# Kernel tuning notes

Hardware: AMD Instinct MI355X
Metric: run time of the kernel (lower is better)

Reference implementation:

```python
import jax, jax.numpy as jnp
import numpy as np

H = 16
QK_DIM = 1024
EPS = 1e-5


def setup_inputs() -> dict:
    key = jax.random.key(0)
    ks = jax.random.split(key, 5)
    B, N, M, D = 2, 2048, 2048, 1024
    x = jax.random.normal(ks[0], (B, N, D), jnp.float32)
    context = jax.random.normal(ks[1], (B, M, D), jnp.float32)
    Wq = jax.random.normal(ks[2], (QK_DIM, D), jnp.float32) * (D ** -0.5)
    Wkv = jax.random.normal(ks[3], (QK_DIM + 1024, D), jnp.float32) * (D ** -0.5)
    Wtalk = jax.random.normal(ks[4], (H, H), jnp.float32) * (H ** -0.5)
    ln_gamma = jnp.ones((H,), jnp.float32)
    ln_beta = jnp.zeros((H,), jnp.float32)
    return {"x": x, "context": context, "Wq": Wq, "Wkv": Wkv,
            "Wtalk": Wtalk, "ln_gamma": ln_gamma, "ln_beta": ln_beta}


def _split_heads(t):
    # b n (h d) -> b h n d
    b, n, hd = t.shape
    return t.reshape(b, n, H, hd // H).transpose(0, 2, 1, 3)


def reference(x, context, Wq, Wkv, Wtalk, ln_gamma, ln_beta):
    q = x @ Wq.T                      # [B,N,QK]
    kv = context @ Wkv.T              # [B,M,QK+V]
    k, v = kv[..., :QK_DIM], kv[..., QK_DIM:]
    q, k, v = _split_heads(q), _split_heads(k), _split_heads(v)
    q = q * (q.shape[-1] ** -0.5)
    scores = jnp.einsum('bhid,bhjd->bhij', q, k)          # [B,H,N,M]
    aw = jax.nn.softmax(scores, axis=-1)
    # talking heads: Linear over head axis then LayerNorm over head axis
    aw = jnp.einsum('bhij,gh->bgij', aw, Wtalk)
    mu = jnp.mean(aw, axis=1, keepdims=True)
    var = jnp.var(aw, axis=1, keepdims=True)
    aw = (aw - mu) * jax.lax.rsqrt(var + EPS)
    aw = aw * ln_gamma[None, :, None, None] + ln_beta[None, :, None, None]
    attn = jnp.einsum('bhij,bhjd->bhid', aw, v)           # [B,H,N,dv]
    b, h, n, d = attn.shape
    return attn.transpose(0, 2, 1, 3).reshape(b, n, h * d)  # [B,N,V]
```

## Files before the change

### kernel.cpp

```cpp
#include <hip/hip_runtime.h>


typedef __attribute__((ext_vector_type(8))) short short8;
typedef __attribute__((ext_vector_type(4))) short short4v;
typedef __attribute__((ext_vector_type(4))) float float4v;
typedef unsigned short u16;

#define MFMA16(a, b, c) __builtin_amdgcn_mfma_f32_16x16x32_bf16((a), (b), (c), 0, 0, 0)

__device__ inline u16 f2bf(float f) {
  unsigned u = __float_as_uint(f);
  u += 0x7FFFu + ((u >> 16) & 1u);
  return (u16)(u >> 16);
}

__global__ __launch_bounds__(256) void cast_bf16(const float* __restrict__ in,
                                                 u16* __restrict__ out, int n) {
  int i = (blockIdx.x * 256 + threadIdx.x) * 8;
  if (i + 8 > n) return;
  float4v f0 = *(const float4v*)(in + i);
  float4v f1 = *(const float4v*)(in + i + 4);
  short8 o;
  o[0] = (short)f2bf(f0[0]); o[1] = (short)f2bf(f0[1]);
  o[2] = (short)f2bf(f0[2]); o[3] = (short)f2bf(f0[3]);
  o[4] = (short)f2bf(f1[0]); o[5] = (short)f2bf(f1[1]);
  o[6] = (short)f2bf(f1[2]); o[7] = (short)f2bf(f1[3]);
  *(short8*)(out + i) = o;
}

template <int MODE>
__global__ __launch_bounds__(256, 4) void gemm_bt(const u16* __restrict__ A,
                                                  const u16* __restrict__ W,
                                                  u16* __restrict__ out0,
                                                  u16* __restrict__ out1) {
  __shared__ u16 As[64][40];
  __shared__ u16 Ws[64][40];
  const int t = threadIdx.x;
  const int wave = t >> 6, l = t & 63, l15 = l & 15, lq = l >> 4;
  const int r0 = blockIdx.x * 64, c0 = blockIdx.y * 64;
  const int srow = t >> 2, sch = t & 3;
  const u16* ag = A + (r0 + srow) * 1024 + sch * 8;
  const u16* wg = W + (c0 + srow) * 1024 + sch * 8;

  float4v acc[4];
#pragma unroll
  for (int i = 0; i < 4; ++i) acc[i] = (float4v){0.f, 0.f, 0.f, 0.f};

  short8 av = *(const short8*)ag;
  short8 wv = *(const short8*)wg;
  for (int kt = 0; kt < 32; ++kt) {
    __syncthreads();
    *(short8*)&As[srow][sch * 8] = av;
    *(short8*)&Ws[srow][sch * 8] = wv;
    __syncthreads();
    if (kt < 31) {
      av = *(const short8*)(ag + (kt + 1) * 32);
      wv = *(const short8*)(wg + (kt + 1) * 32);
    }
    short8 af = *(const short8*)&As[wave * 16 + l15][lq * 8];
#pragma unroll
    for (int fn = 0; fn < 4; ++fn) {
      short8 bf = *(const short8*)&Ws[fn * 16 + l15][lq * 8];
      acc[fn] = MFMA16(af, bf, acc[fn]);
    }
  }
#pragma unroll
  for (int fn = 0; fn < 4; ++fn) {
#pragma unroll
    for (int r = 0; r < 4; ++r) {
      int row = r0 + wave * 16 + lq * 4 + r;
      int col = c0 + fn * 16 + l15;
      int b = row >> 11, n = row & 2047;
      float v = acc[fn][r];
      if (MODE == 0) {
        v *= 0.125f;
        int h = col >> 6, d = col & 63;
        out0[(((b * 16 + h) * 2048 + n) << 6) + d] = f2bf(v);
      } else {
        if (col < 1024) {
          int h = col >> 6, d = col & 63;
          out0[(((b * 16 + h) * 2048 + n) << 6) + d] = f2bf(v);
        } else {
          int cc = col - 1024;
          int h = cc >> 6, d = cc & 63;
          out1[(((b * 16 + h) * 2048 + n) << 6) + d] = f2bf(v);
        }
      }
    }
  }
}

__global__ __launch_bounds__(256) void transpose_v(const u16* __restrict__ vh,
                                                   u16* __restrict__ vt) {
  __shared__ u16 tile[64][72];
  const int t = threadIdx.x;
  const int j0 = blockIdx.x * 64, h = blockIdx.y, b = blockIdx.z;
  const u16* src = vh + (((b * 16 + h) * 2048 + j0) << 6);
  int row = t >> 2, c = t & 3;
  short8 v0 = *(const short8*)(src + row * 64 + c * 8);
  short8 v1 = *(const short8*)(src + row * 64 + (c + 4) * 8);
  *(short8*)&tile[row][c * 8] = v0;
  *(short8*)&tile[row][(c + 4) * 8] = v1;
  __syncthreads();
  int d = t >> 2, jc = t & 3;
  short8 o0, o1;
#pragma unroll
  for (int jj = 0; jj < 8; ++jj) o0[jj] = (short)tile[jc * 16 + jj][d];
#pragma unroll
  for (int jj = 0; jj < 8; ++jj) o1[jj] = (short)tile[jc * 16 + 8 + jj][d];
  u16* dst = vt + ((b * 16 + h) * 64 + d) * 2048 + j0 + jc * 16;
  *(short8*)dst = o0;
  *(short8*)(dst + 8) = o1;
}

__global__ __launch_bounds__(1024) void attn_fused(
    const u16* __restrict__ qh, const u16* __restrict__ kh,
    const u16* __restrict__ vt, const float* __restrict__ wtalk,
    const float* __restrict__ gamma, const float* __restrict__ beta,
    float* __restrict__ out) {
  __shared__ u16 P_lds[2][512 * 36];
  __shared__ u16 Y_lds[2][16 * 16 * 36];

  const int tid = threadIdx.x;
  const int wv = tid >> 6;
  const int l = tid & 63, l15 = l & 15, lq = l >> 4;
  const int i0 = blockIdx.x * 16;
  const int b = blockIdx.y;
  const int bh = b * 16 + wv;

  {
    u16* pz = &P_lds[0][0];
    for (int z = tid; z < 2 * 512 * 36; z += 1024) pz[z] = 0;
  }

  short8 wfrag;
#pragma unroll
  for (int t8 = 0; t8 < 8; ++t8) {
    int h = lq * 8 + t8;
    float wval = (h < 16) ? wtalk[l15 * 16 + h] : 0.f;
    wfrag[t8] = (short)f2bf(wval);
  }
  float gam[4], bet[4];
#pragma unroll
  for (int r = 0; r < 4; ++r) {
    gam[r] = gamma[lq * 4 + r];
    bet[r] = beta[lq * 4 + r];
  }

  const u16* qbase = qh + ((bh * 2048 + i0) << 6);
  short8 qf0 = *(const short8*)(qbase + l15 * 64 + lq * 8);
  short8 qf1 = *(const short8*)(qbase + l15 * 64 + 32 + lq * 8);
  const u16* kbase = kh + ((bh * 2048) << 6);
  const u16* vbase = vt + (bh * 64) * 2048;

  __syncthreads();

  float ps0 = 0.f, ps1 = 0.f, ps2 = 0.f, ps3 = 0.f;
  short8 k00 = *(const short8*)(kbase + l15 * 64 + lq * 8);
  short8 k01 = *(const short8*)(kbase + l15 * 64 + 32 + lq * 8);
  short8 k10 = *(const short8*)(kbase + (16 + l15) * 64 + lq * 8);
  short8 k11 = *(const short8*)(kbase + (16 + l15) * 64 + 32 + lq * 8);
  for (int jt = 0; jt < 64; ++jt) {
    short8 n00, n01, n10, n11;
    if (jt < 63) {
      const u16* kp = kbase + (((jt + 1) * 32) << 6);
      n00 = *(const short8*)(kp + l15 * 64 + lq * 8);
      n01 = *(const short8*)(kp + l15 * 64 + 32 + lq * 8);
      n10 = *(const short8*)(kp + (16 + l15) * 64 + lq * 8);
      n11 = *(const short8*)(kp + (16 + l15) * 64 + 32 + lq * 8);
    }
    float4v s0 = {0.f, 0.f, 0.f, 0.f}, s1 = {0.f, 0.f, 0.f, 0.f};
    s0 = MFMA16(qf0, k00, s0);
    s0 = MFMA16(qf1, k01, s0);
    s1 = MFMA16(qf0, k10, s1);
    s1 = MFMA16(qf1, k11, s1);
    ps0 += __expf(s0[0]) + __expf(s1[0]);
    ps1 += __expf(s0[1]) + __expf(s1[1]);
    ps2 += __expf(s0[2]) + __expf(s1[2]);
    ps3 += __expf(s0[3]) + __expf(s1[3]);
    k00 = n00; k01 = n01; k10 = n10; k11 = n11;
  }
#pragma unroll
  for (int d = 1; d < 16; d <<= 1) {
    ps0 += __shfl_xor(ps0, d);
    ps1 += __shfl_xor(ps1, d);
    ps2 += __shfl_xor(ps2, d);
    ps3 += __shfl_xor(ps3, d);
  }
  float bc[4];
  bc[0] = -logf(ps0); bc[1] = -logf(ps1);
  bc[2] = -logf(ps2); bc[3] = -logf(ps3);

  float4v acc0 = {0.f, 0.f, 0.f, 0.f}, acc1 = acc0, acc2 = acc0, acc3 = acc0;
  short8 kc00 = *(const short8*)(kbase + l15 * 64 + lq * 8);
  short8 kc01 = *(const short8*)(kbase + l15 * 64 + 32 + lq * 8);
  short8 kc10 = *(const short8*)(kbase + (16 + l15) * 64 + lq * 8);
  short8 kc11 = *(const short8*)(kbase + (16 + l15) * 64 + 32 + lq * 8);
  short8 v0, v1, v2, v3;

  for (int jt = 0; jt <= 64; ++jt) {
    const int buf = jt & 1, pbuf = (jt - 1) & 1;
    if (jt >= 1) {
      const u16* vp = vbase + (jt - 1) * 32 + lq * 8;
      v0 = *(const short8*)(vp + (l15) * 2048);
      v1 = *(const short8*)(vp + (16 + l15) * 2048);
      v2 = *(const short8*)(vp + (32 + l15) * 2048);
      v3 = *(const short8*)(vp + (48 + l15) * 2048);
    }
    short8 kn00, kn01, kn10, kn11;
    if (jt + 1 < 64) {
      const u16* kp = kbase + (((jt + 1) * 32) << 6);
      kn00 = *(const short8*)(kp + l15 * 64 + lq * 8);
      kn01 = *(const short8*)(kp + l15 * 64 + 32 + lq * 8);
      kn10 = *(const short8*)(kp + (16 + l15) * 64 + lq * 8);
      kn11 = *(const short8*)(kp + (16 + l15) * 64 + 32 + lq * 8);
    }
    if (jt < 64) {
      float4v s0 = {0.f, 0.f, 0.f, 0.f}, s1 = {0.f, 0.f, 0.f, 0.f};
      s0 = MFMA16(qf0, kc00, s0);
      s0 = MFMA16(qf1, kc01, s0);
      s1 = MFMA16(qf0, kc10, s1);
      s1 = MFMA16(qf1, kc11, s1);
      int ebase = (lq * 4) * 32 + l15;
#pragma unroll
      for (int r = 0; r < 4; ++r) {
        float p0 = __expf(s0[r] + bc[r]);
        float p1 = __expf(s1[r] + bc[r]);
        P_lds[buf][(ebase + r * 32) * 36 + wv] = f2bf(p0);
        P_lds[buf][(ebase + r * 32 + 16) * 36 + wv] = f2bf(p1);
      }
    }
    __syncthreads();
    if (jt < 64) {
      float4v t0 = {0.f, 0.f, 0.f, 0.f}, t1 = {0.f, 0.f, 0.f, 0.f};
      {
        int e00 = wv * 32 + l15;
        int e10 = wv * 32 + 16 + l15;
        const u16* p0p = &P_lds[buf][e00 * 36 + lq * 8];
        const u16* p1p = &P_lds[buf][e10 * 36 + lq * 8];
        short4v x0 = *(const short4v*)p0p;
        short4v x1 = *(const short4v*)(p0p + 4);
        short4v y0 = *(const short4v*)p1p;
        short4v y1 = *(const short4v*)(p1p + 4);
        short8 pb0 = __builtin_shufflevector(x0, x1, 0, 1, 2, 3, 4, 5, 6, 7);
        short8 pb1 = __builtin_shufflevector(y0, y1, 0, 1, 2, 3, 4, 5, 6, 7);
        t0 = MFMA16(wfrag, pb0, t0);
        t1 = MFMA16(wfrag, pb1, t1);
      }
#pragma unroll
      for (int c2 = 0; c2 < 2; ++c2) {
        float4v tt = c2 ? t1 : t0;
        float sum = tt[0] + tt[1] + tt[2] + tt[3];
        sum += __shfl_xor(sum, 16);
        sum += __shfl_xor(sum, 32);
        float mu = sum * 0.0625f;
        float ss = tt[0] * tt[0] + tt[1] * tt[1] + tt[2] * tt[2] + tt[3] * tt[3];
        ss += __shfl_xor(ss, 16);
        ss += __shfl_xor(ss, 32);
        float var = ss * 0.0625f - mu * mu;
        float rs = rsqrtf(var + 1e-5f);
#pragma unroll
        for (int r = 0; r < 4; ++r) {
          float y = (tt[r] - mu) * rs * gam[r] + bet[r];
          Y_lds[buf][((lq * 4 + r) * 16 + wv) * 36 + c2 * 16 + l15] = f2bf(y);
        }
      }
    }
    if (jt >= 1) {
      short8 yf = *(const short8*)&Y_lds[pbuf][(wv * 16 + l15) * 36 + lq * 8];
      acc0 = MFMA16(yf, v0, acc0);
      acc1 = MFMA16(yf, v1, acc1);
      acc2 = MFMA16(yf, v2, acc2);
      acc3 = MFMA16(yf, v3, acc3);
    }
    kc00 = kn00; kc01 = kn01; kc10 = kn10; kc11 = kn11;
  }
  float* ob = out + (b * 2048 + i0) * 1024 + wv * 64;
#pragma unroll
  for (int r = 0; r < 4; ++r) {
    float* orow = ob + (lq * 4 + r) * 1024;
    orow[l15] = acc0[r];
    orow[16 + l15] = acc1[r];
    orow[32 + l15] = acc2[r];
    orow[48 + l15] = acc3[r];
  }
}

extern "C" void kernel_launch(void* const* d_in, const int* in_sizes, int n_in,
                              void* d_out, int out_size, void* d_ws,
                              size_t ws_size, hipStream_t stream) {
  const float* x = (const float*)d_in[0];
  const float* ctx = (const float*)d_in[1];
  const float* Wq = (const float*)d_in[2];
  const float* Wkv = (const float*)d_in[3];
  const float* Wtalk = (const float*)d_in[4];
  const float* gam = (const float*)d_in[5];
  const float* bet = (const float*)d_in[6];
  float* out = (float*)d_out;

  u16* xb = (u16*)d_ws;
  u16* cb = xb + 4194304;
  u16* wqb = cb + 4194304;
  u16* wkvb = wqb + 1048576;
  u16* qhb = wkvb + 2097152;
  u16* khb = qhb + 4194304;
  u16* vhb = khb + 4194304;
  u16* vtb = vhb + 4194304;

  cast_bf16<<<2048, 256, 0, stream>>>(x, xb, 4194304);
  cast_bf16<<<2048, 256, 0, stream>>>(ctx, cb, 4194304);
  cast_bf16<<<512, 256, 0, stream>>>(Wq, wqb, 1048576);
  cast_bf16<<<1024, 256, 0, stream>>>(Wkv, wkvb, 2097152);

  gemm_bt<0><<<dim3(64, 16), 256, 0, stream>>>(xb, wqb, qhb, nullptr);
  gemm_bt<1><<<dim3(64, 32), 256, 0, stream>>>(cb, wkvb, khb, vhb);

  transpose_v<<<dim3(32, 16, 2), 256, 0, stream>>>(vhb, vtb);

  attn_fused<<<dim3(128, 2), 1024, 0, stream>>>(qhb, khb, vtb, Wtalk, gam, bet,
                                                out);
}
```

Measured before the change: 507.1 us.

## Split attention into denominator and pass-2 kernels with key-range split-K and atomics

The fused attention kernel becomes two kernels. The first computes softmax denominators over half the key range per block and accumulates them with atomicAdd. The second does the probability, talking-heads and layernorm, and PV pass per key half, accumulating output with atomics into a memset buffer. This doubles the grid so more CUs are busy. It also folds log2e into the Q scale so exp2 can be used, and shrinks the talking-heads MFMA to a K=16 variant with a smaller P buffer. The cost is extra memsets, float atomics on the output, and nondeterministic summation order.

```diff
diff --git a/kernel.cpp b/kernel.cpp
--- a/kernel.cpp
+++ b/kernel.cpp
@@ -7,12 +7,15 @@
 typedef unsigned short u16;
 
 #define MFMA16(a, b, c) __builtin_amdgcn_mfma_f32_16x16x32_bf16((a), (b), (c), 0, 0, 0)
+#define MFMA16K16(a, b, c) __builtin_amdgcn_mfma_f32_16x16x16bf16_1k((a), (b), (c), 0, 0, 0)
 
 __device__ inline u16 f2bf(float f) {
   unsigned u = __float_as_uint(f);
   u += 0x7FFFu + ((u >> 16) & 1u);
   return (u16)(u >> 16);
 }
+
+__device__ inline float fexp2(float x) { return __builtin_amdgcn_exp2f(x); }
 
 __global__ __launch_bounds__(256) void cast_bf16(const float* __restrict__ in,
                                                  u16* __restrict__ out, int n) {
@@ -73,7 +76,7 @@
       int b = row >> 11, n = row & 2047;
       float v = acc[fn][r];
       if (MODE == 0) {
-        v *= 0.125f;
+        v *= 0.125f * 1.44269504088896f;
         int h = col >> 6, d = col & 63;
         out0[(((b * 16 + h) * 2048 + n) << 6) + d] = f2bf(v);
       } else {
@@ -113,56 +116,30 @@
   *(short8*)(dst + 8) = o1;
 }
 
-__global__ __launch_bounds__(1024) void attn_fused(
+__global__ __launch_bounds__(1024, 8) void attn_denom(
     const u16* __restrict__ qh, const u16* __restrict__ kh,
-    const u16* __restrict__ vt, const float* __restrict__ wtalk,
-    const float* __restrict__ gamma, const float* __restrict__ beta,
-    float* __restrict__ out) {
-  __shared__ u16 P_lds[2][512 * 36];
-  __shared__ u16 Y_lds[2][16 * 16 * 36];
-
+    float* __restrict__ lsum) {
   const int tid = threadIdx.x;
   const int wv = tid >> 6;
   const int l = tid & 63, l15 = l & 15, lq = l >> 4;
   const int i0 = blockIdx.x * 16;
-  const int b = blockIdx.y;
+  const int jh = blockIdx.y;
+  const int b = blockIdx.z;
   const int bh = b * 16 + wv;
-
-  {
-    u16* pz = &P_lds[0][0];
-    for (int z = tid; z < 2 * 512 * 36; z += 1024) pz[z] = 0;
-  }
-
-  short8 wfrag;
-#pragma unroll
-  for (int t8 = 0; t8 < 8; ++t8) {
-    int h = lq * 8 + t8;
-    float wval = (h < 16) ? wtalk[l15 * 16 + h] : 0.f;
-    wfrag[t8] = (short)f2bf(wval);
-  }
-  float gam[4], bet[4];
-#pragma unroll
-  for (int r = 0; r < 4; ++r) {
-    gam[r] = gamma[lq * 4 + r];
-    bet[r] = beta[lq * 4 + r];
-  }
 
   const u16* qbase = qh + ((bh * 2048 + i0) << 6);
   short8 qf0 = *(const short8*)(qbase + l15 * 64 + lq * 8);
   short8 qf1 = *(const short8*)(qbase + l15 * 64 + 32 + lq * 8);
-  const u16* kbase = kh + ((bh * 2048) << 6);
-  const u16* vbase = vt + (bh * 64) * 2048;
-
-  __syncthreads();
+  const u16* kbase = kh + ((bh * 2048 + jh * 1024) << 6);
 
   float ps0 = 0.f, ps1 = 0.f, ps2 = 0.f, ps3 = 0.f;
   short8 k00 = *(const short8*)(kbase + l15 * 64 + lq * 8);
   short8 k01 = *(const short8*)(kbase + l15 * 64 + 32 + lq * 8);
   short8 k10 = *(const short8*)(kbase + (16 + l15) * 64 + lq * 8);
   short8 k11 = *(const short8*)(kbase + (16 + l15) * 64 + 32 + lq * 8);
-  for (int jt = 0; jt < 64; ++jt) {
+  for (int jt = 0; jt < 32; ++jt) {
     short8 n00, n01, n10, n11;
-    if (jt < 63) {
+    if (jt < 31) {
       const u16* kp = kbase + (((jt + 1) * 32) << 6);
       n00 = *(const short8*)(kp + l15 * 64 + lq * 8);
       n01 = *(const short8*)(kp + l15 * 64 + 32 + lq * 8);
@@ -174,10 +151,10 @@
     s0 = MFMA16(qf1, k01, s0);
     s1 = MFMA16(qf0, k10, s1);
     s1 = MFMA16(qf1, k11, s1);
-    ps0 += __expf(s0[0]) + __expf(s1[0]);
-    ps1 += __expf(s0[1]) + __expf(s1[1]);
-    ps2 += __expf(s0[2]) + __expf(s1[2]);
-    ps3 += __expf(s0[3]) + __expf(s1[3]);
+    ps0 += fexp2(s0[0]) + fexp2(s1[0]);
+    ps1 += fexp2(s0[1]) + fexp2(s1[1]);
+    ps2 += fexp2(s0[2]) + fexp2(s1[2]);
+    ps3 += fexp2(s0[3]) + fexp2(s1[3]);
     k00 = n00; k01 = n01; k10 = n10; k11 = n11;
   }
 #pragma unroll
@@ -187,9 +164,52 @@
     ps2 += __shfl_xor(ps2, d);
     ps3 += __shfl_xor(ps3, d);
   }
+  if (l15 == 0) {
+    float* lp = lsum + bh * 2048 + i0 + lq * 4;
+    atomicAdd(lp + 0, ps0);
+    atomicAdd(lp + 1, ps1);
+    atomicAdd(lp + 2, ps2);
+    atomicAdd(lp + 3, ps3);
+  }
+}
+
+__global__ __launch_bounds__(1024, 8) void attn_pass2(
+    const u16* __restrict__ qh, const u16* __restrict__ kh,
+    const u16* __restrict__ vt, const float* __restrict__ wtalk,
+    const float* __restrict__ gamma, const float* __restrict__ beta,
+    const float* __restrict__ lsum, float* __restrict__ out) {
+  __shared__ u16 P_lds[2][512 * 18];
+  __shared__ u16 Y_lds[2][16 * 16 * 36];
+
+  const int tid = threadIdx.x;
+  const int wv = tid >> 6;
+  const int l = tid & 63, l15 = l & 15, lq = l >> 4;
+  const int i0 = blockIdx.x * 16;
+  const int jh = blockIdx.y;
+  const int b = blockIdx.z;
+  const int bh = b * 16 + wv;
+
+  short4v wfrag;
+#pragma unroll
+  for (int t4 = 0; t4 < 4; ++t4)
+    wfrag[t4] = (short)f2bf(wtalk[l15 * 16 + lq * 4 + t4]);
+  float gam[4], bet[4];
+#pragma unroll
+  for (int r = 0; r < 4; ++r) {
+    gam[r] = gamma[lq * 4 + r];
+    bet[r] = beta[lq * 4 + r];
+  }
+
+  const u16* qbase = qh + ((bh * 2048 + i0) << 6);
+  short8 qf0 = *(const short8*)(qbase + l15 * 64 + lq * 8);
+  short8 qf1 = *(const short8*)(qbase + l15 * 64 + 32 + lq * 8);
+  const u16* kbase = kh + ((bh * 2048 + jh * 1024) << 6);
+  const u16* vbase = vt + (bh * 64) * 2048 + jh * 1024;
+
   float bc[4];
-  bc[0] = -logf(ps0); bc[1] = -logf(ps1);
-  bc[2] = -logf(ps2); bc[3] = -logf(ps3);
+#pragma unroll
+  for (int r = 0; r < 4; ++r)
+    bc[r] = -__builtin_amdgcn_logf(lsum[bh * 2048 + i0 + lq * 4 + r]);
 
   float4v acc0 = {0.f, 0.f, 0.f, 0.f}, acc1 = acc0, acc2 = acc0, acc3 = acc0;
   short8 kc00 = *(const short8*)(kbase + l15 * 64 + lq * 8);
@@ -198,54 +218,50 @@
   short8 kc11 = *(const short8*)(kbase + (16 + l15) * 64 + 32 + lq * 8);
   short8 v0, v1, v2, v3;
 
-  for (int jt = 0; jt <= 64; ++jt) {
+  for (int jt = 0; jt <= 32; ++jt) {
     const int buf = jt & 1, pbuf = (jt - 1) & 1;
     if (jt >= 1) {
       const u16* vp = vbase + (jt - 1) * 32 + lq * 8;
-      v0 = *(const short8*)(vp + (l15) * 2048);
+      v0 = *(const short8*)(vp + (l15)*2048);
       v1 = *(const short8*)(vp + (16 + l15) * 2048);
       v2 = *(const short8*)(vp + (32 + l15) * 2048);
       v3 = *(const short8*)(vp + (48 + l15) * 2048);
     }
     short8 kn00, kn01, kn10, kn11;
-    if (jt + 1 < 64) {
+    if (jt + 1 < 32) {
       const u16* kp = kbase + (((jt + 1) * 32) << 6);
       kn00 = *(const short8*)(kp + l15 * 64 + lq * 8);
       kn01 = *(const short8*)(kp + l15 * 64 + 32 + lq * 8);
       kn10 = *(const short8*)(kp + (16 + l15) * 64 + lq * 8);
       kn11 = *(const short8*)(kp + (16 + l15) * 64 + 32 + lq * 8);
     }
-    if (jt < 64) {
+    if (jt < 32) {
       float4v s0 = {0.f, 0.f, 0.f, 0.f}, s1 = {0.f, 0.f, 0.f, 0.f};
       s0 = MFMA16(qf0, kc00, s0);
       s0 = MFMA16(qf1, kc01, s0);
       s1 = MFMA16(qf0, kc10, s1);
       s1 = MFMA16(qf1, kc11, s1);
-      int ebase = (lq * 4) * 32 + l15;
+      int ebase = lq * 128 + l15;
 #pragma unroll
       for (int r = 0; r < 4; ++r) {
-        float p0 = __expf(s0[r] + bc[r]);
-        float p1 = __expf(s1[r] + bc[r]);
-        P_lds[buf][(ebase + r * 32) * 36 + wv] = f2bf(p0);
-        P_lds[buf][(ebase + r * 32 + 16) * 36 + wv] = f2bf(p1);
+        float p0 = fexp2(s0[r] + bc[r]);
+        float p1 = fexp2(s1[r] + bc[r]);
+        P_lds[buf][(ebase + r * 32) * 18 + wv] = f2bf(p0);
+        P_lds[buf][(ebase + r * 32 + 16) * 18 + wv] = f2bf(p1);
       }
     }
     __syncthreads();
-    if (jt < 64) {
+    if (jt < 32) {
       float4v t0 = {0.f, 0.f, 0.f, 0.f}, t1 = {0.f, 0.f, 0.f, 0.f};
       {
-        int e00 = wv * 32 + l15;
-        int e10 = wv * 32 + 16 + l15;
-        const u16* p0p = &P_lds[buf][e00 * 36 + lq * 8];
-        const u16* p1p = &P_lds[buf][e10 * 36 + lq * 8];
-        short4v x0 = *(const short4v*)p0p;
-        short4v x1 = *(const short4v*)(p0p + 4);
-        short4v y0 = *(const short4v*)p1p;
-        short4v y1 = *(const short4v*)(p1p + 4);
-        short8 pb0 = __builtin_shufflevector(x0, x1, 0, 1, 2, 3, 4, 5, 6, 7);
-        short8 pb1 = __builtin_shufflevector(y0, y1, 0, 1, 2, 3, 4, 5, 6, 7);
-        t0 = MFMA16(wfrag, pb0, t0);
-        t1 = MFMA16(wfrag, pb1, t1);
+        const u16* prow = &P_lds[buf][(wv * 32 + l15) * 18 + (lq << 2)];
+        union { int i2[2]; short4v s4; } u0, u1;
+        u0.i2[0] = *(const int*)(prow);
+        u0.i2[1] = *(const int*)(prow + 2);
+        u1.i2[0] = *(const int*)(prow + 16 * 18);
+        u1.i2[1] = *(const int*)(prow + 16 * 18 + 2);
+        t0 = MFMA16K16(wfrag, u0.s4, t0);
+        t1 = MFMA16K16(wfrag, u1.s4, t1);
       }
 #pragma unroll
       for (int c2 = 0; c2 < 2; ++c2) {
@@ -279,10 +295,10 @@
 #pragma unroll
   for (int r = 0; r < 4; ++r) {
     float* orow = ob + (lq * 4 + r) * 1024;
-    orow[l15] = acc0[r];
-    orow[16 + l15] = acc1[r];
-    orow[32 + l15] = acc2[r];
-    orow[48 + l15] = acc3[r];
+    atomicAdd(orow + l15, acc0[r]);
+    atomicAdd(orow + 16 + l15, acc1[r]);
+    atomicAdd(orow + 32 + l15, acc2[r]);
+    atomicAdd(orow + 48 + l15, acc3[r]);
   }
 }
 
@@ -306,6 +322,10 @@
   u16* khb = qhb + 4194304;
   u16* vhb = khb + 4194304;
   u16* vtb = vhb + 4194304;
+  float* lsum = (float*)(vtb + 4194304);
+
+  hipMemsetAsync(lsum, 0, 2 * 16 * 2048 * sizeof(float), stream);
+  hipMemsetAsync(out, 0, 2 * 2048 * 1024 * sizeof(float), stream);
 
   cast_bf16<<<2048, 256, 0, stream>>>(x, xb, 4194304);
   cast_bf16<<<2048, 256, 0, stream>>>(ctx, cb, 4194304);
@@ -317,6 +337,7 @@
 
   transpose_v<<<dim3(32, 16, 2), 256, 0, stream>>>(vhb, vtb);
 
-  attn_fused<<<dim3(128, 2), 1024, 0, stream>>>(qhb, khb, vtb, Wtalk, gam, bet,
-                                                out);
-}
+  attn_denom<<<dim3(128, 2, 2), 1024, 0, stream>>>(qhb, khb, lsum);
+  attn_pass2<<<dim3(128, 2, 2), 1024, 0, stream>>>(qhb, khb, vtb, Wtalk, gam,
+                                                   bet, lsum, out);
+}
```

Result: slower. 864.0 us (+70.4%).

## Unfuse attention into QK-exp, talking-heads LN, and PV GEMM kernels over query chunks

Applied to the files above, without the earlier changes.

Replaces the single fused attention kernel, which computed scores twice (once for the softmax denominator, once for the output) with heavy per-tile syncs, with three kernels run over four query chunks. The first writes bf16 exp2 scores to a scratch buffer and accumulates row sums atomically. The second normalises, applies talking heads and LayerNorm elementwise in place. The third is a tiled GEMM against transposed V. The exp is moved to base 2 by folding log2(e) into the Q scaling. This removes the duplicated QK work and the low-parallelism fused loop, at the cost of materialising large score tensors in global memory and adding launches. Softmax is done without max subtraction, which was already the case before.

```diff
diff --git a/kernel.cpp b/kernel.cpp
--- a/kernel.cpp
+++ b/kernel.cpp
@@ -13,6 +13,10 @@
   u += 0x7FFFu + ((u >> 16) & 1u);
   return (u16)(u >> 16);
 }
+__device__ inline float bf2f(u16 u) {
+  return __uint_as_float(((unsigned)u) << 16);
+}
+__device__ inline float fexp2(float x) { return __builtin_amdgcn_exp2f(x); }
 
 __global__ __launch_bounds__(256) void cast_bf16(const float* __restrict__ in,
                                                  u16* __restrict__ out, int n) {
@@ -73,7 +77,7 @@
       int b = row >> 11, n = row & 2047;
       float v = acc[fn][r];
       if (MODE == 0) {
-        v *= 0.125f;
+        v *= 0.125f * 1.44269504088896f;
         int h = col >> 6, d = col & 63;
         out0[(((b * 16 + h) * 2048 + n) << 6) + d] = f2bf(v);
       } else {
@@ -113,176 +117,160 @@
   *(short8*)(dst + 8) = o1;
 }
 
-__global__ __launch_bounds__(1024) void attn_fused(
-    const u16* __restrict__ qh, const u16* __restrict__ kh,
-    const u16* __restrict__ vt, const float* __restrict__ wtalk,
-    const float* __restrict__ gamma, const float* __restrict__ beta,
-    float* __restrict__ out) {
-  __shared__ u16 P_lds[2][512 * 36];
-  __shared__ u16 Y_lds[2][16 * 16 * 36];
-
+__global__ __launch_bounds__(256) void qk_exp(const u16* __restrict__ qh,
+                                              const u16* __restrict__ kh,
+                                              u16* __restrict__ E,
+                                              float* __restrict__ lsum,
+                                              int i_base) {
+  const int t = threadIdx.x;
+  const int w = t >> 6, l = t & 63, l15 = l & 15, lq = l >> 4;
+  const int it = blockIdx.x;
+  const int jt = blockIdx.y;
+  const int bh = blockIdx.z;
+  const int i0w = it * 64 + w * 16;
+  const int ig = i_base + i0w;
+  const int j0 = jt * 64;
+
+  const u16* qb = qh + (size_t)(bh * 2048 + ig + l15) * 64 + lq * 8;
+  short8 qf0 = *(const short8*)qb;
+  short8 qf1 = *(const short8*)(qb + 32);
+  const u16* kb = kh + (size_t)(bh * 2048 + j0 + l15) * 64 + lq * 8;
+
+  float4v s[4];
+#pragma unroll
+  for (int fn = 0; fn < 4; ++fn) {
+    short8 k0 = *(const short8*)(kb + fn * 16 * 64);
+    short8 k1 = *(const short8*)(kb + fn * 16 * 64 + 32);
+    float4v a = {0.f, 0.f, 0.f, 0.f};
+    a = MFMA16(k0, qf0, a);
+    a = MFMA16(k1, qf1, a);
+    s[fn] = a;
+  }
+
+  u16* eb = E + ((size_t)(bh * 512 + i0w + l15)) * 2048 + j0 + lq * 4;
+  float rs = 0.f;
+#pragma unroll
+  for (int fn = 0; fn < 4; ++fn) {
+    short4v pk;
+#pragma unroll
+    for (int r = 0; r < 4; ++r) {
+      u16 ev = f2bf(fexp2(s[fn][r]));
+      pk[r] = (short)ev;
+      rs += bf2f(ev);
+    }
+    *(short4v*)(eb + fn * 16) = pk;
+  }
+  rs += __shfl_xor(rs, 16);
+  rs += __shfl_xor(rs, 32);
+  if (l < 16) atomicAdd(lsum + (size_t)bh * 2048 + ig + (l - l15) + l15, rs);
+}
+
+__global__ __launch_bounds__(256) void talk_ln(u16* ey,
+                                               const float* __restrict__ lsum,
+                                               const float* __restrict__ wtalk,
+                                               const float* __restrict__ gamma,
+                                               const float* __restrict__ beta,
+                                               int i_base) {
+  __shared__ float wt[256];
+  __shared__ float invl[16], ga[16], be[16];
   const int tid = threadIdx.x;
-  const int wv = tid >> 6;
-  const int l = tid & 63, l15 = l & 15, lq = l >> 4;
-  const int i0 = blockIdx.x * 16;
-  const int b = blockIdx.y;
-  const int bh = b * 16 + wv;
-
-  {
-    u16* pz = &P_lds[0][0];
-    for (int z = tid; z < 2 * 512 * 36; z += 1024) pz[z] = 0;
-  }
-
-  short8 wfrag;
-#pragma unroll
-  for (int t8 = 0; t8 < 8; ++t8) {
-    int h = lq * 8 + t8;
-    float wval = (h < 16) ? wtalk[l15 * 16 + h] : 0.f;
-    wfrag[t8] = (short)f2bf(wval);
-  }
-  float gam[4], bet[4];
-#pragma unroll
-  for (int r = 0; r < 4; ++r) {
-    gam[r] = gamma[lq * 4 + r];
-    bet[r] = beta[lq * 4 + r];
-  }
-
-  const u16* qbase = qh + ((bh * 2048 + i0) << 6);
-  short8 qf0 = *(const short8*)(qbase + l15 * 64 + lq * 8);
-  short8 qf1 = *(const short8*)(qbase + l15 * 64 + 32 + lq * 8);
-  const u16* kbase = kh + ((bh * 2048) << 6);
-  const u16* vbase = vt + (bh * 64) * 2048;
-
+  const int jc = blockIdx.x, iq = blockIdx.y, b = blockIdx.z;
+  const int ig = i_base + iq;
+  wt[tid] = wtalk[tid];
+  if (tid < 16) {
+    invl[tid] = 1.f / lsum[(size_t)(b * 16 + tid) * 2048 + ig];
+    ga[tid] = gamma[tid];
+    be[tid] = beta[tid];
+  }
   __syncthreads();
 
-  float ps0 = 0.f, ps1 = 0.f, ps2 = 0.f, ps3 = 0.f;
-  short8 k00 = *(const short8*)(kbase + l15 * 64 + lq * 8);
-  short8 k01 = *(const short8*)(kbase + l15 * 64 + 32 + lq * 8);
-  short8 k10 = *(const short8*)(kbase + (16 + l15) * 64 + lq * 8);
-  short8 k11 = *(const short8*)(kbase + (16 + l15) * 64 + 32 + lq * 8);
-  for (int jt = 0; jt < 64; ++jt) {
-    short8 n00, n01, n10, n11;
-    if (jt < 63) {
-      const u16* kp = kbase + (((jt + 1) * 32) << 6);
-      n00 = *(const short8*)(kp + l15 * 64 + lq * 8);
-      n01 = *(const short8*)(kp + l15 * 64 + 32 + lq * 8);
-      n10 = *(const short8*)(kp + (16 + l15) * 64 + lq * 8);
-      n11 = *(const short8*)(kp + (16 + l15) * 64 + 32 + lq * 8);
-    }
-    float4v s0 = {0.f, 0.f, 0.f, 0.f}, s1 = {0.f, 0.f, 0.f, 0.f};
-    s0 = MFMA16(qf0, k00, s0);
-    s0 = MFMA16(qf1, k01, s0);
-    s1 = MFMA16(qf0, k10, s1);
-    s1 = MFMA16(qf1, k11, s1);
-    ps0 += __expf(s0[0]) + __expf(s1[0]);
-    ps1 += __expf(s0[1]) + __expf(s1[1]);
-    ps2 += __expf(s0[2]) + __expf(s1[2]);
-    ps3 += __expf(s0[3]) + __expf(s1[3]);
-    k00 = n00; k01 = n01; k10 = n10; k11 = n11;
-  }
-#pragma unroll
-  for (int d = 1; d < 16; d <<= 1) {
-    ps0 += __shfl_xor(ps0, d);
-    ps1 += __shfl_xor(ps1, d);
-    ps2 += __shfl_xor(ps2, d);
-    ps3 += __shfl_xor(ps3, d);
-  }
-  float bc[4];
-  bc[0] = -logf(ps0); bc[1] = -logf(ps1);
-  bc[2] = -logf(ps2); bc[3] = -logf(ps3);
-
-  float4v acc0 = {0.f, 0.f, 0.f, 0.f}, acc1 = acc0, acc2 = acc0, acc3 = acc0;
-  short8 kc00 = *(const short8*)(kbase + l15 * 64 + lq * 8);
-  short8 kc01 = *(const short8*)(kbase + l15 * 64 + 32 + lq * 8);
-  short8 kc10 = *(const short8*)(kbase + (16 + l15) * 64 + lq * 8);
-  short8 kc11 = *(const short8*)(kbase + (16 + l15) * 64 + 32 + lq * 8);
-  short8 v0, v1, v2, v3;
-
-  for (int jt = 0; jt <= 64; ++jt) {
-    const int buf = jt & 1, pbuf = (jt - 1) & 1;
-    if (jt >= 1) {
-      const u16* vp = vbase + (jt - 1) * 32 + lq * 8;
-      v0 = *(const short8*)(vp + (l15) * 2048);
-      v1 = *(const short8*)(vp + (16 + l15) * 2048);
-      v2 = *(const short8*)(vp + (32 + l15) * 2048);
-      v3 = *(const short8*)(vp + (48 + l15) * 2048);
-    }
-    short8 kn00, kn01, kn10, kn11;
-    if (jt + 1 < 64) {
-      const u16* kp = kbase + (((jt + 1) * 32) << 6);
-      kn00 = *(const short8*)(kp + l15 * 64 + lq * 8);
-      kn01 = *(const short8*)(kp + l15 * 64 + 32 + lq * 8);
-      kn10 = *(const short8*)(kp + (16 + l15) * 64 + lq * 8);
-      kn11 = *(const short8*)(kp + (16 + l15) * 64 + 32 + lq * 8);
-    }
-    if (jt < 64) {
-      float4v s0 = {0.f, 0.f, 0.f, 0.f}, s1 = {0.f, 0.f, 0.f, 0.f};
-      s0 = MFMA16(qf0, kc00, s0);
-      s0 = MFMA16(qf1, kc01, s0);
-      s1 = MFMA16(qf0, kc10, s1);
-      s1 = MFMA16(qf1, kc11, s1);
-      int ebase = (lq * 4) * 32 + l15;
-#pragma unroll
-      for (int r = 0; r < 4; ++r) {
-        float p0 = __expf(s0[r] + bc[r]);
-        float p1 = __expf(s1[r] + bc[r]);
-        P_lds[buf][(ebase + r * 32) * 36 + wv] = f2bf(p0);
-        P_lds[buf][(ebase + r * 32 + 16) * 36 + wv] = f2bf(p1);
-      }
-    }
+  const int j = jc * 512 + tid * 2;
+  const size_t base = ((size_t)(b * 16) * 512 + iq) * 2048 + j;
+  const size_t hstride = (size_t)512 * 2048;
+
+  float p0[16], p1[16];
+#pragma unroll
+  for (int h = 0; h < 16; ++h) {
+    unsigned u = *(const unsigned*)(ey + base + h * hstride);
+    float il = invl[h];
+    p0[h] = bf2f((u16)(u & 0xffffu)) * il;
+    p1[h] = bf2f((u16)(u >> 16)) * il;
+  }
+  float t0[16], t1[16];
+#pragma unroll
+  for (int g = 0; g < 16; ++g) { t0[g] = 0.f; t1[g] = 0.f; }
+#pragma unroll
+  for (int h = 0; h < 16; ++h) {
+#pragma unroll
+    for (int g = 0; g < 16; ++g) {
+      float wv = wt[g * 16 + h];
+      t0[g] += wv * p0[h];
+      t1[g] += wv * p1[h];
+    }
+  }
+  float mu0 = 0.f, mu1 = 0.f, ss0 = 0.f, ss1 = 0.f;
+#pragma unroll
+  for (int g = 0; g < 16; ++g) {
+    mu0 += t0[g]; ss0 += t0[g] * t0[g];
+    mu1 += t1[g]; ss1 += t1[g] * t1[g];
+  }
+  mu0 *= 0.0625f; mu1 *= 0.0625f;
+  float rv0 = rsqrtf(ss0 * 0.0625f - mu0 * mu0 + 1e-5f);
+  float rv1 = rsqrtf(ss1 * 0.0625f - mu1 * mu1 + 1e-5f);
+#pragma unroll
+  for (int g = 0; g < 16; ++g) {
+    float y0 = (t0[g] - mu0) * rv0 * ga[g] + be[g];
+    float y1 = (t1[g] - mu1) * rv1 * ga[g] + be[g];
+    unsigned o = (unsigned)f2bf(y0) | ((unsigned)f2bf(y1) << 16);
+    *(unsigned*)(ey + base + g * hstride) = o;
+  }
+}
+
+__global__ __launch_bounds__(256, 4) void pv_gemm(const u16* __restrict__ Y,
+                                                  const u16* __restrict__ VT,
+                                                  float* __restrict__ out,
+                                                  int i_base) {
+  __shared__ u16 As[64][40];
+  __shared__ u16 Ws[64][40];
+  const int t = threadIdx.x;
+  const int wave = t >> 6, l = t & 63, l15 = l & 15, lq = l >> 4;
+  const int r0 = blockIdx.x * 64;
+  const int bg = blockIdx.y;
+  const int srow = t >> 2, sch = t & 3;
+  const u16* ag = Y + ((size_t)bg * 512 + r0 + srow) * 2048 + sch * 8;
+  const u16* wg = VT + ((size_t)bg * 64 + srow) * 2048 + sch * 8;
+
+  float4v acc[4];
+#pragma unroll
+  for (int i = 0; i < 4; ++i) acc[i] = (float4v){0.f, 0.f, 0.f, 0.f};
+
+  short8 av = *(const short8*)ag;
+  short8 wv = *(const short8*)wg;
+  for (int kt = 0; kt < 64; ++kt) {
     __syncthreads();
-    if (jt < 64) {
-      float4v t0 = {0.f, 0.f, 0.f, 0.f}, t1 = {0.f, 0.f, 0.f, 0.f};
-      {
-        int e00 = wv * 32 + l15;
-        int e10 = wv * 32 + 16 + l15;
-        const u16* p0p = &P_lds[buf][e00 * 36 + lq * 8];
-        const u16* p1p = &P_lds[buf][e10 * 36 + lq * 8];
-        short4v x0 = *(const short4v*)p0p;
-        short4v x1 = *(const short4v*)(p0p + 4);
-        short4v y0 = *(const short4v*)p1p;
-        short4v y1 = *(const short4v*)(p1p + 4);
-        short8 pb0 = __builtin_shufflevector(x0, x1, 0, 1, 2, 3, 4, 5, 6, 7);
-        short8 pb1 = __builtin_shufflevector(y0, y1, 0, 1, 2, 3, 4, 5, 6, 7);
-        t0 = MFMA16(wfrag, pb0, t0);
-        t1 = MFMA16(wfrag, pb1, t1);
-      }
-#pragma unroll
-      for (int c2 = 0; c2 < 2; ++c2) {
-        float4v tt = c2 ? t1 : t0;
-        float sum = tt[0] + tt[1] + tt[2] + tt[3];
-        sum += __shfl_xor(sum, 16);
-        sum += __shfl_xor(sum, 32);
-        float mu = sum * 0.0625f;
-        float ss = tt[0] * tt[0] + tt[1] * tt[1] + tt[2] * tt[2] + tt[3] * tt[3];
-        ss += __shfl_xor(ss, 16);
-        ss += __shfl_xor(ss, 32);
-        float var = ss * 0.0625f - mu * mu;
-        float rs = rsqrtf(var + 1e-5f);
-#pragma unroll
-        for (int r = 0; r < 4; ++r) {
-          float y = (tt[r] - mu) * rs * gam[r] + bet[r];
-          Y_lds[buf][((lq * 4 + r) * 16 + wv) * 36 + c2 * 16 + l15] = f2bf(y);
-        }
-      }
-    }
-    if (jt >= 1) {
-      short8 yf = *(const short8*)&Y_lds[pbuf][(wv * 16 + l15) * 36 + lq * 8];
-      acc0 = MFMA16(yf, v0, acc0);
-      acc1 = MFMA16(yf, v1, acc1);
-      acc2 = MFMA16(yf, v2, acc2);
-      acc3 = MFMA16(yf, v3, acc3);
-    }
-    kc00 = kn00; kc01 = kn01; kc10 = kn10; kc11 = kn11;
-  }
-  float* ob = out + (b * 2048 + i0) * 1024 + wv * 64;
-#pragma unroll
-  for (int r = 0; r < 4; ++r) {
-    float* orow = ob + (lq * 4 + r) * 1024;
-    orow[l15] = acc0[r];
-    orow[16 + l15] = acc1[r];
-    orow[32 + l15] = acc2[r];
-    orow[48 + l15] = acc3[r];
+    *(short8*)&As[srow][sch * 8] = av;
+    *(short8*)&Ws[srow][sch * 8] = wv;
+    __syncthreads();
+    if (kt < 63) {
+      av = *(const short8*)(ag + (kt + 1) * 32);
+      wv = *(const short8*)(wg + (kt + 1) * 32);
+    }
+    short8 af = *(const short8*)&As[wave * 16 + l15][lq * 8];
+#pragma unroll
+    for (int fn = 0; fn < 4; ++fn) {
+      short8 bf = *(const short8*)&Ws[fn * 16 + l15][lq * 8];
+      acc[fn] = MFMA16(af, bf, acc[fn]);
+    }
+  }
+  const int b = bg >> 4, g = bg & 15;
+#pragma unroll
+  for (int fn = 0; fn < 4; ++fn) {
+#pragma unroll
+    for (int r = 0; r < 4; ++r) {
+      int row = i_base + r0 + wave * 16 + lq * 4 + r;
+      int col = g * 64 + fn * 16 + l15;
+      out[((size_t)b * 2048 + row) * 1024 + col] = acc[fn][r];
+    }
   }
 }
 
@@ -298,14 +286,20 @@
   const float* bet = (const float*)d_in[6];
   float* out = (float*)d_out;
 
-  u16* xb = (u16*)d_ws;
-  u16* cb = xb + 4194304;
-  u16* wqb = cb + 4194304;
-  u16* wkvb = wqb + 1048576;
-  u16* qhb = wkvb + 2097152;
-  u16* khb = qhb + 4194304;
-  u16* vhb = khb + 4194304;
-  u16* vtb = vhb + 4194304;
+  u16* ws = (u16*)d_ws;
+  u16* qhb = ws;
+  u16* khb = ws + 4194304;
+  u16* vtb = ws + 8388608;
+  float* lsum = (float*)(ws + 12582912);
+  u16* scr = ws + 12845056;
+  u16* xb = scr;
+  u16* cb = scr + 4194304;
+  u16* wqb = scr + 8388608;
+  u16* wkvb = scr + 9437184;
+  u16* vhb = scr + 11534336;
+  u16* E = scr;
+
+  hipMemsetAsync(lsum, 0, 65536 * sizeof(float), stream);
 
   cast_bf16<<<2048, 256, 0, stream>>>(x, xb, 4194304);
   cast_bf16<<<2048, 256, 0, stream>>>(ctx, cb, 4194304);
@@ -317,6 +311,11 @@
 
   transpose_v<<<dim3(32, 16, 2), 256, 0, stream>>>(vhb, vtb);
 
-  attn_fused<<<dim3(128, 2), 1024, 0, stream>>>(qhb, khb, vtb, Wtalk, gam, bet,
-                                                out);
-}
+  for (int q = 0; q < 4; ++q) {
+    int i_base = q * 512;
+    qk_exp<<<dim3(8, 32, 32), 256, 0, stream>>>(qhb, khb, E, lsum, i_base);
+    talk_ln<<<dim3(4, 512, 2), 256, 0, stream>>>(E, lsum, Wtalk, gam, bet,
+                                                 i_base);
+    pv_gemm<<<dim3(8, 32), 256, 0, stream>>>(E, vtb, out, i_base);
+  }
+}
```

After: 622.2 us. 22.7% more time.
